# Kernel tuning notes

Hardware: AMD Instinct MI355X
Metric: run time of the kernel (lower is better)

Reference implementation:

```python
import jax, jax.numpy as jnp
import numpy as np

B, C, H, W, S = 4, 16, 256, 256, 100
OMEGA2 = (0.01 * S) ** 2  # alpha=0.01, n_spixels=100 -> 1.0
EPS = 1e-32


def setup_inputs() -> dict:
    key = jax.random.key(0)
    ks = jax.random.split(key, 7)
    pf = jax.random.normal(ks[0], (B, C, H, W), jnp.float32)
    spf1 = jax.random.normal(ks[1], (B, C, S), jnp.float32)
    spf2 = jax.random.normal(ks[2], (B, C, S), jnp.float32)
    Q1 = jax.random.uniform(ks[3], (B, S, H * W), jnp.float32)
    Q2 = jax.random.uniform(ks[4], (B, S, H * W), jnp.float32)
    w_ds = jax.random.normal(ks[5], (2, C, 3, 3), jnp.float32) * 0.05
    b_ds = jnp.zeros((2,), jnp.float32)
    return {"pf": pf, "spf1": spf1, "spf2": spf2, "Q1": Q1, "Q2": Q2,
            "w_ds": w_ds, "b_ds": b_ds}


def _affinity_pool(pf_flat, spf, Q):
    """merge=True branch: pairwise superpixel affinities, then affinity-weighted
    normalized pixel->superpixel pooling.
    pf_flat: [B,C,N], spf: [B,C,S] (detached), Q: [B,S,N] (detached)."""
    d = spf[:, :, None, :] - spf[:, :, :, None]          # [B,C,S,S]
    rels = jnp.exp(-jnp.sum(d * d, axis=1) / OMEGA2)      # [B,S,S]
    coeffs = jnp.einsum('bst,btn->bsn', rels, Q)          # map_sp2p(rels, Q)
    num = jnp.einsum('bcn,bsn->bcs', pf_flat, coeffs)     # pf @ coeffs^T
    return num / (jnp.sum(coeffs, axis=-1)[:, None, :] + EPS)  # [B,C,S]


def reference(pf, spf1, spf2, Q1, Q2, w_ds, b_ds):
    b, c, h, w = pf.shape
    pf_flat = pf.reshape(b, c, h * w)
    spf1n = _affinity_pool(pf_flat, spf1, Q1)
    spf2n = _affinity_pool(pf_flat, spf2, Q2)
    # map_sp2p: superpixel features back to pixels
    pf1 = jnp.einsum('bcs,bsn->bcn', spf1n, Q1).reshape(b, c, h, w)
    pf2 = jnp.einsum('bcs,bsn->bcn', spf2n, Q2).reshape(b, c, h, w)
    pf_sp = pf1 + pf2
    # conv_ds: Conv3x3(out_ch, 2), no bn/act
    prob_ds = jax.lax.conv_general_dilated(
        pf_sp, w_ds, window_strides=(1, 1), padding='SAME',
        dimension_numbers=('NCHW', 'OIHW', 'NCHW')) + b_ds[None, :, None, None]
    return prob_ds
```

## Files before the change

### kernel.cpp

```cpp
#include <hip/hip_runtime.h>

#define BB 4
#define CC 16
#define HH 256
#define WW 256
#define NN (HH*WW)
#define SS 100
#define EPSV 1e-32f

#define PQ_OFF    0u
#define SPFN_OFF  13600u
#define PFSP_OFF  26400u
#define PPART_OFF PFSP_OFF

__device__ __forceinline__ float dot4(const float4& a, const float4& b) {
    return a.x * b.x + a.y * b.y + a.z * b.z + a.w * b.w;
}
__device__ __forceinline__ float sum4(const float4& a) {
    return a.x + a.y + a.z + a.w;
}

#define DPPQP(x, ctrl) __int_as_float(__builtin_amdgcn_update_dpp( \
    0, __float_as_int(x), ctrl, 0xF, 0xF, true))

#define PIN4(p) asm volatile("" : "+v"(p.x), "+v"(p.y), "+v"(p.z), "+v"(p.w));
#define PIN_PF  PIN4(p00) PIN4(p01) PIN4(p10) PIN4(p11) \
                PIN4(p20) PIN4(p21) PIN4(p30) PIN4(p31) \
                PIN4(p40) PIN4(p41) PIN4(p50) PIN4(p51) \
                PIN4(p60) PIN4(p61) PIN4(p70) PIN4(p71)

#define P1_STEP(Q0, Q1v, sidx) { \
    float t0 = dot4(p00,Q0)+dot4(p01,Q1v); \
    float t1 = dot4(p10,Q0)+dot4(p11,Q1v); \
    float t2 = dot4(p20,Q0)+dot4(p21,Q1v); \
    float t3 = dot4(p30,Q0)+dot4(p31,Q1v); \
    float t4 = dot4(p40,Q0)+dot4(p41,Q1v); \
    float t5 = dot4(p50,Q0)+dot4(p51,Q1v); \
    float t6 = dot4(p60,Q0)+dot4(p61,Q1v); \
    float t7 = dot4(p70,Q0)+dot4(p71,Q1v); \
    t0 += DPPQP(t0,0xB1); t1 += DPPQP(t1,0xB1); \
    t2 += DPPQP(t2,0xB1); t3 += DPPQP(t3,0xB1); \
    t4 += DPPQP(t4,0xB1); t5 += DPPQP(t5,0xB1); \
    t6 += DPPQP(t6,0xB1); t7 += DPPQP(t7,0xB1); \
    float u0 = odd ? t1 : t0; float u1 = odd ? t3 : t2; \
    float u2 = odd ? t5 : t4; float u3 = odd ? t7 : t6; \
    u0 += DPPQP(u0,0x4E); u1 += DPPQP(u1,0x4E); \
    u2 += DPPQP(u2,0x4E); u3 += DPPQP(u3,0x4E); \
    float w0 = hi2 ? u1 : u0; float w1 = hi2 ? u3 : u2; \
    w0 += DPPQP(w0,0x114); w1 += DPPQP(w1,0x114); \
    w0 += DPPQP(w0,0x118); w1 += DPPQP(w1,0x118); \
    w0 += __shfl_xor(w0,32); w1 += __shfl_xor(w1,32); \
    if (ch8 == 0) { \
        float qv = sum4(Q0)+sum4(Q1v); \
        qv += DPPQP(qv,0xB1); qv += DPPQP(qv,0x4E); \
        qv += DPPQP(qv,0x114); qv += DPPQP(qv,0x118); \
        qv += __shfl_xor(qv,32); \
        if ((lane & 15) == 15 && lane < 32) \
            sout[(size_t)(sidx)*34 + (lane>>4)*17 + 16] = qv; \
    } \
    if ((lane & 15) >= 12 && lane < 32) { \
        float* o = sout + (size_t)(sidx)*34 + (lane>>4)*17 + ch8 + (lane & 3); \
        o[0] = w0; o[4] = w1; \
    } \
}

__global__ __launch_bounds__(256, 2) void k_pass1(const float* __restrict__ pf,
                                                  const float* __restrict__ Q1,
                                                  const float* __restrict__ Q2,
                                                  float* __restrict__ ws) {
    int tid = threadIdx.x, wid = tid >> 6, lane = tid & 63;
    int h  = wid & 1;
    int nh = wid >> 1;
    int win = blockIdx.x;
    int sp  = blockIdx.y;
    int bq  = blockIdx.z;
    int b = bq >> 1, q = bq & 1;
    bool odd = lane & 1;
    bool hi2 = lane & 2;
    int ch8 = h * 8;

    int nbase = win * 1024 + nh * 512 + lane * 4;
    const float* qptr = (q ? Q2 : Q1) + (size_t)b * SS * NN
                        + (size_t)(sp * 20) * NN + nbase;
    const float* PF   = pf + (size_t)b * CC * NN + (size_t)ch8 * NN + nbase;

    float4 p00 = *(const float4*)(PF + (size_t)0 * NN);
    float4 p01 = *(const float4*)(PF + (size_t)0 * NN + 256);
    float4 p10 = *(const float4*)(PF + (size_t)1 * NN);
    float4 p11 = *(const float4*)(PF + (size_t)1 * NN + 256);
    float4 p20 = *(const float4*)(PF + (size_t)2 * NN);
    float4 p21 = *(const float4*)(PF + (size_t)2 * NN + 256);
    float4 p30 = *(const float4*)(PF + (size_t)3 * NN);
    float4 p31 = *(const float4*)(PF + (size_t)3 * NN + 256);
    float4 p40 = *(const float4*)(PF + (size_t)4 * NN);
    float4 p41 = *(const float4*)(PF + (size_t)4 * NN + 256);
    float4 p50 = *(const float4*)(PF + (size_t)5 * NN);
    float4 p51 = *(const float4*)(PF + (size_t)5 * NN + 256);
    float4 p60 = *(const float4*)(PF + (size_t)6 * NN);
    float4 p61 = *(const float4*)(PF + (size_t)6 * NN + 256);
    float4 p70 = *(const float4*)(PF + (size_t)7 * NN);
    float4 p71 = *(const float4*)(PF + (size_t)7 * NN + 256);

    float* sout = ws + PPART_OFF
                + (size_t)((bq * 64 + win) * 2 + nh) * 3400
                + (size_t)(sp * 20) * 34;

    #pragma unroll
    for (int s = 0; s < 20; ++s) {
        PIN_PF
        float4 Qa = *(const float4*)(qptr + (size_t)s * NN);
        float4 Qb = *(const float4*)(qptr + (size_t)s * NN + 256);
        P1_STEP(Qa, Qb, s)
    }
}

__global__ __launch_bounds__(256) void k_reduceP(float* __restrict__ ws) {
    int sgc = blockIdx.x;
    int bq  = blockIdx.y;
    int tid = threadIdx.x;
    if (tid < 170) {
        int sl = tid / 17, c = tid % 17;
        const float* p = ws + PPART_OFF + (size_t)(bq * 128) * 3400
                       + (size_t)(sgc * 10 + sl) * 34 + c;
        float a0 = 0.f, a1 = 0.f, a2 = 0.f, a3 = 0.f;
        #pragma unroll 4
        for (int hw = 0; hw < 128; hw += 2) {
            a0 += p[(size_t)hw * 3400];
            a1 += p[(size_t)hw * 3400 + 17];
            a2 += p[(size_t)(hw + 1) * 3400];
            a3 += p[(size_t)(hw + 1) * 3400 + 17];
        }
        ws[PQ_OFF + (size_t)(bq * 100 + sgc * 10 + sl) * 17 + c]
            = (a0 + a1) + (a2 + a3);
    }
}

__global__ __launch_bounds__(256) void k_finalize(const float* __restrict__ spf1,
                                                  const float* __restrict__ spf2,
                                                  float* __restrict__ ws) {
    int sq = blockIdx.x;
    int bq = blockIdx.y;
    int b = bq >> 1, q = bq & 1;
    __shared__ float sp[CC][SS];
    __shared__ float rl[25][SS + 1];
    __shared__ float Pl[CC * SS];
    __shared__ float qs[SS];
    __shared__ float den[25];
    int tid = threadIdx.x;

    const float* spf = (q ? spf2 : spf1) + (size_t)b * CC * SS;
    for (int i = tid; i < CC * SS; i += 256) sp[i / SS][i % SS] = spf[i];
    const float* pq = ws + PQ_OFF + (size_t)bq * 100 * 17;
    for (int idx = tid; idx < CC * SS; idx += 256) {
        int c = idx / SS, t = idx % SS;
        Pl[idx] = pq[(size_t)t * 17 + c];
    }
    if (tid < SS) qs[tid] = pq[(size_t)tid * 17 + 16];
    __syncthreads();
    for (int i = tid; i < 25 * SS; i += 256) {
        int sl = i / SS, t = i % SS;
        int s = sq * 25 + sl;
        float d2 = 0.f;
        #pragma unroll
        for (int c = 0; c < CC; ++c) {
            float d = sp[c][t] - sp[c][s];
            d2 += d * d;
        }
        rl[sl][t] = expf(-d2);
    }
    __syncthreads();
    if (tid < 25) {
        float a = 0.f;
        for (int t = 0; t < SS; ++t) a += rl[tid][t] * qs[t];
        den[tid] = a + EPSV;
    }
    __syncthreads();
    float* sout = ws + SPFN_OFF + (size_t)bq * SS * CC;
    for (int idx = tid; idx < 25 * CC; idx += 256) {
        int sl = idx / CC, c = idx % CC;
        float a = 0.f;
        for (int t = 0; t < SS; ++t) a += rl[sl][t] * Pl[c * SS + t];
        sout[(size_t)(sq * 25 + sl) * CC + c] = a / den[sl];
    }
}

#define P2STEP(V1, V2, s) { \
    _Pragma("unroll") for (int g = 0; g < 4; ++g) { \
        float4 s1 = *(const float4*)(sp1 + (s) * CC + g * 4); \
        float4 s2 = *(const float4*)(sp2 + (s) * CC + g * 4); \
        acc[g*4+0].x += s1.x*V1.x + s2.x*V2.x; \
        acc[g*4+0].y += s1.x*V1.y + s2.x*V2.y; \
        acc[g*4+1].x += s1.y*V1.x + s2.y*V2.x; \
        acc[g*4+1].y += s1.y*V1.y + s2.y*V2.y; \
        acc[g*4+2].x += s1.z*V1.x + s2.z*V2.x; \
        acc[g*4+2].y += s1.z*V1.y + s2.z*V2.y; \
        acc[g*4+3].x += s1.w*V1.x + s2.w*V2.x; \
        acc[g*4+3].y += s1.w*V1.y + s2.w*V2.y; } }

__global__ __launch_bounds__(256) void k_pass2(const float* __restrict__ Q1,
                                               const float* __restrict__ Q2,
                                               float* __restrict__ ws) {
    int blk = blockIdx.x;
    int b   = blockIdx.y;
    int tid = threadIdx.x;
    int n = blk * 512 + tid * 2;
    const float* q1p = Q1 + (size_t)b * SS * NN + n;
    const float* q2p = Q2 + (size_t)b * SS * NN + n;
    const float* sp1 = ws + SPFN_OFF + (size_t)(b * 2 + 0) * SS * CC;
    const float* sp2 = ws + SPFN_OFF + (size_t)(b * 2 + 1) * SS * CC;
    float2 acc[CC];
    #pragma unroll
    for (int c = 0; c < CC; ++c) acc[c] = make_float2(0.f, 0.f);
    float2 A1, A2, B1, B2;
    A1 = *(const float2*)(q1p);
    A2 = *(const float2*)(q2p);
    #pragma unroll 2
    for (int s = 0; s < 98; s += 2) {
        B1 = *(const float2*)(q1p + (size_t)(s + 1) * NN);
        B2 = *(const float2*)(q2p + (size_t)(s + 1) * NN);
        P2STEP(A1, A2, s)
        A1 = *(const float2*)(q1p + (size_t)(s + 2) * NN);
        A2 = *(const float2*)(q2p + (size_t)(s + 2) * NN);
        P2STEP(B1, B2, s + 1)
    }
    B1 = *(const float2*)(q1p + (size_t)99 * NN);
    B2 = *(const float2*)(q2p + (size_t)99 * NN);
    P2STEP(A1, A2, 98)
    P2STEP(B1, B2, 99)
    float* o = ws + PFSP_OFF + (size_t)b * CC * NN + n;
    #pragma unroll
    for (int c = 0; c < CC; ++c)
        *(float2*)(o + (size_t)c * NN) = acc[c];
}

__global__ __launch_bounds__(256) void k_conv(const float* __restrict__ w_ds,
                                              const float* __restrict__ b_ds,
                                              const float* __restrict__ ws,
                                              float* __restrict__ out) {
    int b = blockIdx.y;
    int n = blockIdx.x * 256 + threadIdx.x;
    __shared__ float wl[2][CC][9];
    __shared__ float bl[2];
    for (int i = threadIdx.x; i < 2 * CC * 9; i += 256)
        ((float*)wl)[i] = w_ds[i];
    if (threadIdx.x < 2) bl[threadIdx.x] = b_ds[threadIdx.x];
    __syncthreads();
    int y = n >> 8, x = n & 255;
    const float* base = ws + PFSP_OFF + (size_t)b * CC * NN;
    float a0 = bl[0], a1 = bl[1];
    for (int c = 0; c < CC; ++c) {
        const float* pc = base + (size_t)c * NN;
        #pragma unroll
        for (int dy = -1; dy <= 1; ++dy) {
            int yy = y + dy;
            if (yy < 0 || yy >= HH) continue;
            #pragma unroll
            for (int dx = -1; dx <= 1; ++dx) {
                int xx = x + dx;
                if (xx < 0 || xx >= WW) continue;
                float v = pc[(size_t)yy * WW + xx];
                int k = (dy + 1) * 3 + (dx + 1);
                a0 += v * wl[0][c][k];
                a1 += v * wl[1][c][k];
            }
        }
    }
    out[((size_t)b * 2 + 0) * NN + n] = a0;
    out[((size_t)b * 2 + 1) * NN + n] = a1;
}

extern "C" void kernel_launch(void* const* d_in, const int* in_sizes, int n_in,
                              void* d_out, int out_size, void* d_ws, size_t ws_size,
                              hipStream_t stream) {
    const float* pf   = (const float*)d_in[0];
    const float* spf1 = (const float*)d_in[1];
    const float* spf2 = (const float*)d_in[2];
    const float* Q1   = (const float*)d_in[3];
    const float* Q2   = (const float*)d_in[4];
    const float* w_ds = (const float*)d_in[5];
    const float* b_ds = (const float*)d_in[6];
    float* ws  = (float*)d_ws;
    float* out = (float*)d_out;

    k_pass1<<<dim3(64, 5, 8), 256, 0, stream>>>(pf, Q1, Q2, ws);
    k_reduceP<<<dim3(10, 8), 256, 0, stream>>>(ws);
    k_finalize<<<dim3(4, 8), 256, 0, stream>>>(spf1, spf2, ws);
    k_pass2<<<dim3(128, BB), 256, 0, stream>>>(Q1, Q2, ws);
    k_conv<<<dim3(NN / 256, BB), 256, 0, stream>>>(w_ds, b_ds, ws, out);
}
```

Baseline: 160.9 us.

## Re-split pass1 work across channels, stage superpixel features in LDS for pass2

```diff
diff --git a/kernel.cpp b/kernel.cpp
--- a/kernel.cpp
+++ b/kernel.cpp
@@ -9,8 +9,8 @@
 #define EPSV 1e-32f
 
 #define PQ_OFF    0u
-#define SPFN_OFF  13600u
-#define PFSP_OFF  26400u
+#define SPFN_OFF  27200u
+#define PFSP_OFF  40000u
 #define PPART_OFF PFSP_OFF
 
 __device__ __forceinline__ float dot4(const float4& a, const float4& b) {
@@ -23,45 +23,32 @@
 #define DPPQP(x, ctrl) __int_as_float(__builtin_amdgcn_update_dpp( \
     0, __float_as_int(x), ctrl, 0xF, 0xF, true))
 
-#define PIN4(p) asm volatile("" : "+v"(p.x), "+v"(p.y), "+v"(p.z), "+v"(p.w));
-#define PIN_PF  PIN4(p00) PIN4(p01) PIN4(p10) PIN4(p11) \
-                PIN4(p20) PIN4(p21) PIN4(p30) PIN4(p31) \
-                PIN4(p40) PIN4(p41) PIN4(p50) PIN4(p51) \
-                PIN4(p60) PIN4(p61) PIN4(p70) PIN4(p71)
-
-#define P1_STEP(Q0, Q1v, sidx) { \
-    float t0 = dot4(p00,Q0)+dot4(p01,Q1v); \
-    float t1 = dot4(p10,Q0)+dot4(p11,Q1v); \
-    float t2 = dot4(p20,Q0)+dot4(p21,Q1v); \
-    float t3 = dot4(p30,Q0)+dot4(p31,Q1v); \
-    float t4 = dot4(p40,Q0)+dot4(p41,Q1v); \
-    float t5 = dot4(p50,Q0)+dot4(p51,Q1v); \
-    float t6 = dot4(p60,Q0)+dot4(p61,Q1v); \
-    float t7 = dot4(p70,Q0)+dot4(p71,Q1v); \
+#define ASM_LD4(dst, addr) \
+    asm volatile("global_load_dwordx4 %0, %1, off" : "=v"(dst) : "v"(addr));
+
+#define P1_STEP(QA, QB, sidx) { \
+    float t0 = dot4(p00,QA)+dot4(p01,QB); \
+    float t1 = dot4(p10,QA)+dot4(p11,QB); \
+    float t2 = dot4(p20,QA)+dot4(p21,QB); \
+    float t3 = dot4(p30,QA)+dot4(p31,QB); \
     t0 += DPPQP(t0,0xB1); t1 += DPPQP(t1,0xB1); \
     t2 += DPPQP(t2,0xB1); t3 += DPPQP(t3,0xB1); \
-    t4 += DPPQP(t4,0xB1); t5 += DPPQP(t5,0xB1); \
-    t6 += DPPQP(t6,0xB1); t7 += DPPQP(t7,0xB1); \
     float u0 = odd ? t1 : t0; float u1 = odd ? t3 : t2; \
-    float u2 = odd ? t5 : t4; float u3 = odd ? t7 : t6; \
     u0 += DPPQP(u0,0x4E); u1 += DPPQP(u1,0x4E); \
-    u2 += DPPQP(u2,0x4E); u3 += DPPQP(u3,0x4E); \
-    float w0 = hi2 ? u1 : u0; float w1 = hi2 ? u3 : u2; \
-    w0 += DPPQP(w0,0x114); w1 += DPPQP(w1,0x114); \
-    w0 += DPPQP(w0,0x118); w1 += DPPQP(w1,0x118); \
-    w0 += __shfl_xor(w0,32); w1 += __shfl_xor(w1,32); \
-    if (ch8 == 0) { \
-        float qv = sum4(Q0)+sum4(Q1v); \
-        qv += DPPQP(qv,0xB1); qv += DPPQP(qv,0x4E); \
+    float w = hi2 ? u1 : u0; \
+    w += DPPQP(w,0x114); \
+    w += DPPQP(w,0x118); \
+    w += __shfl_xor(w,16); \
+    if (wid == 0) { \
+        float qv = sum4(QA)+sum4(QB); \
+        qv += DPPQP(qv,0x111); qv += DPPQP(qv,0x112); \
         qv += DPPQP(qv,0x114); qv += DPPQP(qv,0x118); \
-        qv += __shfl_xor(qv,32); \
-        if ((lane & 15) == 15 && lane < 32) \
-            sout[(size_t)(sidx)*34 + (lane>>4)*17 + 16] = qv; \
+        qv += __shfl_xor(qv,16); \
+        if ((lane & 31) == 15) \
+            sout[(size_t)(sidx)*34 + (lane>>5)*17 + 16] = qv; \
     } \
-    if ((lane & 15) >= 12 && lane < 32) { \
-        float* o = sout + (size_t)(sidx)*34 + (lane>>4)*17 + ch8 + (lane & 3); \
-        o[0] = w0; o[4] = w1; \
-    } \
+    if ((lane & 15) >= 12 && (lane & 16) == 0) \
+        sout[(size_t)(sidx)*34 + (lane>>5)*17 + ch4 + (lane & 3)] = w; \
 }
 
 __global__ __launch_bounds__(256, 2) void k_pass1(const float* __restrict__ pf,
@@ -69,69 +56,64 @@
                                                   const float* __restrict__ Q2,
                                                   float* __restrict__ ws) {
     int tid = threadIdx.x, wid = tid >> 6, lane = tid & 63;
-    int h  = wid & 1;
-    int nh = wid >> 1;
     int win = blockIdx.x;
     int sp  = blockIdx.y;
     int bq  = blockIdx.z;
     int b = bq >> 1, q = bq & 1;
     bool odd = lane & 1;
     bool hi2 = lane & 2;
-    int ch8 = h * 8;
-
-    int nbase = win * 1024 + nh * 512 + lane * 4;
+    int ch4 = wid * 4;
+
+    int nbase = win * 512 + lane * 8;
     const float* qptr = (q ? Q2 : Q1) + (size_t)b * SS * NN
                         + (size_t)(sp * 20) * NN + nbase;
-    const float* PF   = pf + (size_t)b * CC * NN + (size_t)ch8 * NN + nbase;
-
-    float4 p00 = *(const float4*)(PF + (size_t)0 * NN);
-    float4 p01 = *(const float4*)(PF + (size_t)0 * NN + 256);
-    float4 p10 = *(const float4*)(PF + (size_t)1 * NN);
-    float4 p11 = *(const float4*)(PF + (size_t)1 * NN + 256);
-    float4 p20 = *(const float4*)(PF + (size_t)2 * NN);
-    float4 p21 = *(const float4*)(PF + (size_t)2 * NN + 256);
-    float4 p30 = *(const float4*)(PF + (size_t)3 * NN);
-    float4 p31 = *(const float4*)(PF + (size_t)3 * NN + 256);
-    float4 p40 = *(const float4*)(PF + (size_t)4 * NN);
-    float4 p41 = *(const float4*)(PF + (size_t)4 * NN + 256);
-    float4 p50 = *(const float4*)(PF + (size_t)5 * NN);
-    float4 p51 = *(const float4*)(PF + (size_t)5 * NN + 256);
-    float4 p60 = *(const float4*)(PF + (size_t)6 * NN);
-    float4 p61 = *(const float4*)(PF + (size_t)6 * NN + 256);
-    float4 p70 = *(const float4*)(PF + (size_t)7 * NN);
-    float4 p71 = *(const float4*)(PF + (size_t)7 * NN + 256);
+    const float* PF   = pf + (size_t)b * CC * NN + (size_t)ch4 * NN + nbase;
+
+    float4 p00, p01, p10, p11, p20, p21, p30, p31;
+    ASM_LD4(p00, PF)
+    ASM_LD4(p01, PF + 4)
+    ASM_LD4(p10, PF + (size_t)1 * NN)
+    ASM_LD4(p11, PF + (size_t)1 * NN + 4)
+    ASM_LD4(p20, PF + (size_t)2 * NN)
+    ASM_LD4(p21, PF + (size_t)2 * NN + 4)
+    ASM_LD4(p30, PF + (size_t)3 * NN)
+    ASM_LD4(p31, PF + (size_t)3 * NN + 4)
+    asm volatile("s_waitcnt vmcnt(0)" ::: "memory");
 
     float* sout = ws + PPART_OFF
-                + (size_t)((bq * 64 + win) * 2 + nh) * 3400
-                + (size_t)(sp * 20) * 34;
-
+                + ((size_t)(bq * 128 + win) * 100 + sp * 20) * 34;
+
+    float4 Aa, Ab, Ba, Bb;
+    Aa = *(const float4*)(qptr);
+    Ab = *(const float4*)(qptr + 4);
     #pragma unroll
-    for (int s = 0; s < 20; ++s) {
-        PIN_PF
-        float4 Qa = *(const float4*)(qptr + (size_t)s * NN);
-        float4 Qb = *(const float4*)(qptr + (size_t)s * NN + 256);
-        P1_STEP(Qa, Qb, s)
-    }
+    for (int s = 0; s < 18; s += 2) {
+        Ba = *(const float4*)(qptr + (size_t)(s + 1) * NN);
+        Bb = *(const float4*)(qptr + (size_t)(s + 1) * NN + 4);
+        P1_STEP(Aa, Ab, s)
+        Aa = *(const float4*)(qptr + (size_t)(s + 2) * NN);
+        Ab = *(const float4*)(qptr + (size_t)(s + 2) * NN + 4);
+        P1_STEP(Ba, Bb, s + 1)
+    }
+    Ba = *(const float4*)(qptr + (size_t)19 * NN);
+    Bb = *(const float4*)(qptr + (size_t)19 * NN + 4);
+    P1_STEP(Aa, Ab, 18)
+    P1_STEP(Ba, Bb, 19)
 }
 
 __global__ __launch_bounds__(256) void k_reduceP(float* __restrict__ ws) {
-    int sgc = blockIdx.x;
-    int bq  = blockIdx.y;
-    int tid = threadIdx.x;
-    if (tid < 170) {
-        int sl = tid / 17, c = tid % 17;
-        const float* p = ws + PPART_OFF + (size_t)(bq * 128) * 3400
-                       + (size_t)(sgc * 10 + sl) * 34 + c;
-        float a0 = 0.f, a1 = 0.f, a2 = 0.f, a3 = 0.f;
+    int strip = blockIdx.x;
+    int bq    = blockIdx.y;
+    int idx = strip * 256 + threadIdx.x;
+    if (idx < 3400) {
+        const float* pp = ws + PPART_OFF + (size_t)bq * 128 * 3400 + idx;
+        float a0 = 0.f, a1 = 0.f;
         #pragma unroll 4
-        for (int hw = 0; hw < 128; hw += 2) {
-            a0 += p[(size_t)hw * 3400];
-            a1 += p[(size_t)hw * 3400 + 17];
-            a2 += p[(size_t)(hw + 1) * 3400];
-            a3 += p[(size_t)(hw + 1) * 3400 + 17];
+        for (int win = 0; win < 128; win += 2) {
+            a0 += pp[(size_t)win * 3400];
+            a1 += pp[(size_t)(win + 1) * 3400];
         }
-        ws[PQ_OFF + (size_t)(bq * 100 + sgc * 10 + sl) * 17 + c]
-            = (a0 + a1) + (a2 + a3);
+        ws[PQ_OFF + (size_t)bq * 3400 + idx] = a0 + a1;
     }
 }
 
@@ -150,12 +132,12 @@
 
     const float* spf = (q ? spf2 : spf1) + (size_t)b * CC * SS;
     for (int i = tid; i < CC * SS; i += 256) sp[i / SS][i % SS] = spf[i];
-    const float* pq = ws + PQ_OFF + (size_t)bq * 100 * 17;
+    const float* pq = ws + PQ_OFF + (size_t)bq * 3400;
     for (int idx = tid; idx < CC * SS; idx += 256) {
         int c = idx / SS, t = idx % SS;
-        Pl[idx] = pq[(size_t)t * 17 + c];
-    }
-    if (tid < SS) qs[tid] = pq[(size_t)tid * 17 + 16];
+        Pl[idx] = pq[(size_t)t * 34 + c] + pq[(size_t)t * 34 + 17 + c];
+    }
+    if (tid < SS) qs[tid] = pq[(size_t)tid * 34 + 16] + pq[(size_t)tid * 34 + 33];
     __syncthreads();
     for (int i = tid; i < 25 * SS; i += 256) {
         int sl = i / SS, t = i % SS;
@@ -186,8 +168,8 @@
 
 #define P2STEP(V1, V2, s) { \
     _Pragma("unroll") for (int g = 0; g < 4; ++g) { \
-        float4 s1 = *(const float4*)(sp1 + (s) * CC + g * 4); \
-        float4 s2 = *(const float4*)(sp2 + (s) * CC + g * 4); \
+        float4 s1 = *(const float4*)&spl[(0 * SS + (s)) * CC + g * 4]; \
+        float4 s2 = *(const float4*)&spl[(SS + (s)) * CC + g * 4]; \
         acc[g*4+0].x += s1.x*V1.x + s2.x*V2.x; \
         acc[g*4+0].y += s1.x*V1.y + s2.x*V2.y; \
         acc[g*4+1].x += s1.y*V1.x + s2.y*V2.x; \
@@ -197,17 +179,19 @@
         acc[g*4+3].x += s1.w*V1.x + s2.w*V2.x; \
         acc[g*4+3].y += s1.w*V1.y + s2.w*V2.y; } }
 
-__global__ __launch_bounds__(256) void k_pass2(const float* __restrict__ Q1,
+__global__ __launch_bounds__(128) void k_pass2(const float* __restrict__ Q1,
                                                const float* __restrict__ Q2,
                                                float* __restrict__ ws) {
     int blk = blockIdx.x;
     int b   = blockIdx.y;
+    __shared__ float spl[2 * SS * CC];
     int tid = threadIdx.x;
-    int n = blk * 512 + tid * 2;
+    const float* spin = ws + SPFN_OFF + (size_t)b * 2 * SS * CC;
+    for (int idx = tid; idx < 2 * SS * CC; idx += 128) spl[idx] = spin[idx];
+    __syncthreads();
+    int n = blk * 256 + tid * 2;
     const float* q1p = Q1 + (size_t)b * SS * NN + n;
     const float* q2p = Q2 + (size_t)b * SS * NN + n;
-    const float* sp1 = ws + SPFN_OFF + (size_t)(b * 2 + 0) * SS * CC;
-    const float* sp2 = ws + SPFN_OFF + (size_t)(b * 2 + 1) * SS * CC;
     float2 acc[CC];
     #pragma unroll
     for (int c = 0; c < CC; ++c) acc[c] = make_float2(0.f, 0.f);
@@ -282,9 +266,9 @@
     float* ws  = (float*)d_ws;
     float* out = (float*)d_out;
 
-    k_pass1<<<dim3(64, 5, 8), 256, 0, stream>>>(pf, Q1, Q2, ws);
-    k_reduceP<<<dim3(10, 8), 256, 0, stream>>>(ws);
+    k_pass1<<<dim3(128, 5, 8), 256, 0, stream>>>(pf, Q1, Q2, ws);
+    k_reduceP<<<dim3(14, 8), 256, 0, stream>>>(ws);
     k_finalize<<<dim3(4, 8), 256, 0, stream>>>(spf1, spf2, ws);
-    k_pass2<<<dim3(128, BB), 256, 0, stream>>>(Q1, Q2, ws);
+    k_pass2<<<dim3(256, BB), 128, 0, stream>>>(Q1, Q2, ws);
     k_conv<<<dim3(NN / 256, BB), 256, 0, stream>>>(w_ds, b_ds, ws, out);
 }
```

New measurement: 159.4 us. About the same (-0.9%).
